# Kernel optimization log

Hardware: AMD Instinct MI355X
Metric: run time of the kernel (lower is better)

Reference implementation:

```python
import math
import jax, jax.numpy as jnp
import numpy as np

N_HEADS = 8

def setup_inputs() -> dict:
    key = jax.random.key(0)
    k1, k2 = jax.random.split(key)
    b, c, n = 8, 512, 2048  # c = n_heads * d = 8 * 64
    qkv = jax.random.normal(k1, (b, 3 * c, n), dtype=jnp.float32)
    mask = jax.random.uniform(k2, (b, n)) > 0.1
    return {"qkv": qkv, "mask": mask}

def reference(qkv, mask):
    b, width, n = qkv.shape
    m = N_HEADS
    assert width % (3 * m) == 0
    d = width // (3 * m)
    # 'b (m D) n -> (b m) D n' with D = 3d, then split into q, k, v
    x = qkv.reshape(b, m, 3 * d, n).reshape(b * m, 3 * d, n)
    q, k, v = x[:, :d], x[:, d:2 * d], x[:, 2 * d:]
    scale = 1.0 / math.sqrt(math.sqrt(d))
    # (B, i, j) attention logits, B = b*m
    weight = jnp.einsum('Bdi,Bdj->Bij', q * scale, k * scale)
    # mask: 'b j -> (b m) () j'
    mkey = jnp.broadcast_to(mask[:, None, None, :], (b, m, 1, n)).reshape(b * m, 1, n)
    neg = -jnp.finfo(weight.dtype).max
    weight = jnp.where(mkey, weight, neg)
    weight = jax.nn.softmax(weight, axis=-1)
    a = jnp.einsum('Bin,Bdn->Bdi', weight, v)  # (b*m, d, n)
    return a.reshape(b, m, d, n).reshape(b, m * d, n)
```

## Files before the change

### kernel.cpp

```cpp
#include <hip/hip_runtime.h>
#include <hip/hip_bf16.h>


typedef __attribute__((ext_vector_type(8))) short short8;
typedef __attribute__((ext_vector_type(4))) float f32x4;
typedef __attribute__((ext_vector_type(4))) unsigned int u32x4;

#define SEQ 2048
#define DH 64
#define NH 8
#define NHEADS_TOT 64
#define NTILES 32
#define TILE_BYTES 8192
#define IMG_MAT (NHEADS_TOT * NTILES * TILE_BYTES)
#define WS_NEED (3 * (size_t)IMG_MAT + 65536)
#define LOG2E 1.4426950408889634f
#define QSCALE (0.125f * LOG2E)

__device__ __forceinline__ unsigned short f2b(float f) {
  unsigned int u = __float_as_uint(f);
  u += 0x7FFFu + ((u >> 16) & 1u);
  return (unsigned short)(u >> 16);
}
__device__ __forceinline__ unsigned int pk2(float a, float b) {
  return (unsigned int)f2b(a) | ((unsigned int)f2b(b) << 16);
}
__device__ __forceinline__ unsigned int cvtpk(float lo, float hi) {
  unsigned int r;
  asm("v_cvt_pk_bf16_f32 %0, %1, %2" : "=v"(r) : "v"(lo), "v"(hi));
  return r;
}
union pkcast { u32x4 u; short8 s; };

__global__ __launch_bounds__(256)
void qkv_prep(const float* __restrict__ qkv, const void* __restrict__ mraw,
              char* __restrict__ ws) {
  __shared__ float Lf[64 * 68];
  __shared__ float mcol[64];
  __shared__ int flag;
  const int tid = threadIdx.x;
  const int b = blockIdx.x;

  if (b >= 3 * NHEADS_TOT * NTILES) {
    const int bi = b - 3 * NHEADS_TOT * NTILES;
    if (tid == 0) flag = 0;
    __syncthreads();
    const int* mi = (const int*)mraw;
    int bad = 0;
    for (int idx = tid; idx < 4096; idx += 256) {
      int v = mi[idx];
      bad |= (v != 0) & (v != 1);
    }
    if (bad) atomicOr(&flag, 1);
    __syncthreads();
    const bool isByte = (flag != 0);
    unsigned short* mo = (unsigned short*)(ws + 3 * (size_t)IMG_MAT) + bi * SEQ;
    for (int j = tid; j < SEQ; j += 256) {
      bool keep = isByte ? (((const unsigned char*)mraw)[bi * SEQ + j] != 0)
                         : (((const int*)mraw)[bi * SEQ + j] != 0);
      mo[j] = keep ? 0x3F80 : 0;
    }
    return;
  }

  const int m = b / (NHEADS_TOT * NTILES);
  const int rem = b - m * (NHEADS_TOT * NTILES);
  const int head = rem >> 5;
  const int t = rem & 31;
  const int bi = head >> 3, h = head & 7;
  const float* src = qkv + (size_t)bi * (3 * NH * DH * SEQ)
                         + (size_t)h * (3 * DH * SEQ)
                         + (size_t)m * (DH * SEQ);
  char* img = ws + (size_t)m * IMG_MAT + (size_t)(head * NTILES + t) * TILE_BYTES;

  if (m == 2) {
    if (tid == 0) flag = 0;
    __syncthreads();
    const int* mi = (const int*)mraw;
    int bad = 0;
    for (int idx = tid; idx < 4096; idx += 256) {
      int v = mi[idx];
      bad |= (v != 0) & (v != 1);
    }
    if (bad) atomicOr(&flag, 1);
    __syncthreads();
    const bool isByte = (flag != 0);
    if (tid < 64) {
      int j = t * 64 + tid;
      bool keep = isByte ? (((const unsigned char*)mraw)[bi * SEQ + j] != 0)
                         : (((const int*)mraw)[bi * SEQ + j] != 0);
      mcol[tid] = keep ? 1.0f : 0.0f;
    }
  }

  const float qs = (m == 0) ? QSCALE : 1.0f;
  const int trow = tid >> 4;
  const int tj4 = (tid & 15) * 4;
  #pragma unroll
  for (int p = 0; p < 4; ++p) {
    int dd = p * 16 + trow;
    float4 v = *(const float4*)(src + (size_t)dd * SEQ + t * 64 + tj4);
    v.x *= qs; v.y *= qs; v.z *= qs; v.w *= qs;
    *(float4*)(&Lf[dd * 68 + tj4]) = v;
  }
  __syncthreads();

  #pragma unroll
  for (int qq = 0; qq < 2; ++qq) {
    int q = tid * 2 + qq;
    int row = q >> 3;
    int cp = q & 7;
    int c = cp ^ (row & 7);
    unsigned int u[4];
    if (m == 2) {
      #pragma unroll
      for (int e2 = 0; e2 < 4; ++e2) {
        int cc = c * 8 + e2 * 2;
        float a = Lf[row * 68 + cc] * mcol[cc];
        float bb = Lf[row * 68 + cc + 1] * mcol[cc + 1];
        u[e2] = pk2(a, bb);
      }
    } else {
      #pragma unroll
      for (int e2 = 0; e2 < 4; ++e2) {
        float a = Lf[(c * 8 + e2 * 2) * 68 + row];
        float bb = Lf[(c * 8 + e2 * 2 + 1) * 68 + row];
        u[e2] = pk2(a, bb);
      }
    }
    u32x4 uv = { u[0], u[1], u[2], u[3] };
    *(u32x4*)(img + q * 16) = uv;
  }
}

#define KOFF 0
#define VOFF 16384
#define MOFF 32768
#define SMEMB 36864

__device__ __forceinline__ void async16(const void* g, void* l) {
  __builtin_amdgcn_global_load_lds(
      (const __attribute__((address_space(1))) void*)g,
      (__attribute__((address_space(3))) void*)l, 16, 0, 0);
}

__global__ __launch_bounds__(256, 4)
void qkv_attn2(const char* __restrict__ ws, float* __restrict__ out) {
  __shared__ __align__(16) char smem[SMEMB];
  const int tid = threadIdx.x;
  const int w = tid >> 6;
  const int lane = tid & 63;
  const int l15 = lane & 15;
  const int g = lane >> 4;
  const int l7 = l15 & 7;

  const int L = blockIdx.x;
  const int head = (L & 7) * 8 + ((L >> 3) >> 4);
  const int qblk = (L >> 3) & 15;
  const int bi = head >> 3, h = head & 7;

  const char* Qimg = ws + (size_t)(head * NTILES + qblk * 2) * TILE_BYTES;
  const char* Kimg = ws + (size_t)IMG_MAT + (size_t)(head * NTILES) * TILE_BYTES;
  const char* Vimg = ws + 2 * (size_t)IMG_MAT + (size_t)(head * NTILES) * TILE_BYTES;
  const char* m01g = ws + 3 * (size_t)IMG_MAT + (size_t)bi * (SEQ * 2);

  short8 qb[2][2];
  {
    const char* qt = Qimg + (w >> 1) * TILE_BYTES;
    const int rbase = (w & 1) * 32;
    #pragma unroll
    for (int mt = 0; mt < 2; ++mt)
      #pragma unroll
      for (int kk = 0; kk < 2; ++kk) {
        int row = rbase + mt * 16 + l15;
        int cp = (kk * 4 + g) ^ l7;
        qb[mt][kk] = *(const short8*)(qt + row * 128 + cp * 16);
      }
  }

  int kOff[4][2];
  #pragma unroll
  for (int f = 0; f < 4; ++f) {
    int row = 8 * (l15 >> 2) + (l15 & 3) + 4 * (f & 1) + 32 * (f >> 1);
    int r7 = row & 7;
    kOff[f][0] = row * 128 + (((0 + g) ^ r7) * 16);
    kOff[f][1] = row * 128 + (((4 + g) ^ r7) * 16);
  }
  int vOff[4][2];
  #pragma unroll
  for (int nt = 0; nt < 4; ++nt) {
    int vrow = nt * 16 + l15;
    vOff[nt][0] = vrow * 128 + (((0 + g) ^ l7) * 16);
    vOff[nt][1] = vrow * 128 + (((4 + g) ^ l7) * 16);
  }

  const int stOff = (w * 2 * 64 + lane) * 16;

  auto stage = [&](int buf, int tt) {
    const char* kt = Kimg + (size_t)tt * TILE_BYTES + stOff;
    const char* vt = Vimg + (size_t)tt * TILE_BYTES + stOff;
    char* kl = smem + KOFF + buf * 8192 + (w * 2) * 1024;
    char* vl = smem + VOFF + buf * 8192 + (w * 2) * 1024;
    async16(kt, kl);
    async16(kt + 1024, kl + 1024);
    async16(vt, vl);
    async16(vt + 1024, vl + 1024);
  };

  async16(m01g + w * 1024 + lane * 16, smem + MOFF + w * 1024);
  stage(0, 0);
  __syncthreads();

  f32x4 accO[2][4];
  #pragma unroll
  for (int mt = 0; mt < 2; ++mt)
    #pragma unroll
    for (int nt = 0; nt < 4; ++nt)
      accO[mt][nt] = (f32x4){0.f, 0.f, 0.f, 0.f};
  f32x4 accL[2];
  accL[0] = (f32x4){0.f, 0.f, 0.f, 0.f};
  accL[1] = (f32x4){0.f, 0.f, 0.f, 0.f};

  for (int t = 0; t < NTILES; ++t) {
    const int cur = t & 1;
    if (t + 1 < NTILES) stage(cur ^ 1, t + 1);

    const char* Kl = smem + KOFF + cur * 8192;
    f32x4 sAcc[2][4];
    __builtin_amdgcn_s_setprio(1);
    #pragma unroll
    for (int f = 0; f < 4; ++f) {
      short8 kb0 = *(const short8*)(Kl + kOff[f][0]);
      short8 kb1 = *(const short8*)(Kl + kOff[f][1]);
      #pragma unroll
      for (int mt = 0; mt < 2; ++mt) {
        f32x4 z = (f32x4){0.f, 0.f, 0.f, 0.f};
        z = __builtin_amdgcn_mfma_f32_16x16x32_bf16(kb0, qb[mt][0], z, 0, 0, 0);
        z = __builtin_amdgcn_mfma_f32_16x16x32_bf16(kb1, qb[mt][1], z, 0, 0, 0);
        sAcc[mt][f] = z;
      }
    }
    __builtin_amdgcn_s_setprio(0);

    short8 pa[2][2];
    #pragma unroll
    for (int mt = 0; mt < 2; ++mt) {
      float pv[4][4];
      #pragma unroll
      for (int f = 0; f < 4; ++f)
        #pragma unroll
        for (int r = 0; r < 4; ++r)
          pv[f][r] = __builtin_exp2f(sAcc[mt][f][r]);
      pkcast lo, hi;
      lo.u = (u32x4){ cvtpk(pv[0][0], pv[0][1]), cvtpk(pv[0][2], pv[0][3]),
                      cvtpk(pv[1][0], pv[1][1]), cvtpk(pv[1][2], pv[1][3]) };
      hi.u = (u32x4){ cvtpk(pv[2][0], pv[2][1]), cvtpk(pv[2][2], pv[2][3]),
                      cvtpk(pv[3][0], pv[3][1]), cvtpk(pv[3][2], pv[3][3]) };
      pa[mt][0] = lo.s;
      pa[mt][1] = hi.s;
    }

    const char* Ml = smem + MOFF + t * 128;
    short8 mf0 = *(const short8*)(Ml + g * 16);
    short8 mf1 = *(const short8*)(Ml + 64 + g * 16);
    #pragma unroll
    for (int mt = 0; mt < 2; ++mt) {
      accL[mt] = __builtin_amdgcn_mfma_f32_16x16x32_bf16(mf0, pa[mt][0], accL[mt], 0, 0, 0);
      accL[mt] = __builtin_amdgcn_mfma_f32_16x16x32_bf16(mf1, pa[mt][1], accL[mt], 0, 0, 0);
    }

    const char* Vl = smem + VOFF + cur * 8192;
    __builtin_amdgcn_s_setprio(1);
    #pragma unroll
    for (int nt = 0; nt < 4; ++nt) {
      short8 va0 = *(const short8*)(Vl + vOff[nt][0]);
      short8 va1 = *(const short8*)(Vl + vOff[nt][1]);
      #pragma unroll
      for (int mt = 0; mt < 2; ++mt) {
        accO[mt][nt] = __builtin_amdgcn_mfma_f32_16x16x32_bf16(va0, pa[mt][0], accO[mt][nt], 0, 0, 0);
        accO[mt][nt] = __builtin_amdgcn_mfma_f32_16x16x32_bf16(va1, pa[mt][1], accO[mt][nt], 0, 0, 0);
      }
    }
    __builtin_amdgcn_s_setprio(0);
    __syncthreads();
  }

  float* obase = out + (size_t)bi * (NH * DH * SEQ) + (size_t)h * (DH * SEQ);
  const int i0 = qblk * 128 + w * 32;
  #pragma unroll
  for (int mt = 0; mt < 2; ++mt) {
    float rl = 1.0f / accL[mt][0];
    int icol = i0 + mt * 16 + l15;
    #pragma unroll
    for (int nt = 0; nt < 4; ++nt)
      #pragma unroll
      for (int r = 0; r < 4; ++r) {
        int dd = nt * 16 + g * 4 + r;
        obase[(size_t)dd * SEQ + icol] = accO[mt][nt][r] * rl;
      }
  }
}

#define QT0 64
#define KT0 64
#define LDK0 72
#define OFF_QT0 0
#define OFF_KT0 9216
#define OFF_VL0 18432
#define OFF_P0  27648
#define OFF_MB0 36864
#define OFF_L0  37120
#define OFF_FLAG0 37376
#define SMEM_BYTES0 37408
#define NEG_BIG 3.0e38f

__device__ __forceinline__ float b2f(unsigned short s) {
  return __uint_as_float(((unsigned int)s) << 16);
}

__global__ __launch_bounds__(256, 2)
void qkv_attn_fused(const float* __restrict__ qkv,
                    const void* __restrict__ mraw,
                    float* __restrict__ out) {
  __shared__ __align__(16) char smem[SMEM_BYTES0];
  unsigned short* Qt = (unsigned short*)(smem + OFF_QT0);
  unsigned short* Kt = (unsigned short*)(smem + OFF_KT0);
  unsigned short* Vl = (unsigned short*)(smem + OFF_VL0);
  unsigned short* P  = (unsigned short*)(smem + OFF_P0);
  float* mb_lds = (float*)(smem + OFF_MB0);
  float* l_lds  = (float*)(smem + OFF_L0);
  int* flag = (int*)(smem + OFF_FLAG0);

  const int tid  = threadIdx.x;
  const int w    = tid >> 6;
  const int lane = tid & 63;
  const int l15  = lane & 15;
  const int g    = lane >> 4;
  const int dbase = g * 8;

  if (tid == 0) *flag = 0;
  __syncthreads();
  {
    const int* mi = (const int*)mraw;
    int bad = 0;
    for (int idx = tid; idx < 4096; idx += 256) {
      int v = mi[idx];
      bad |= (v != 0) & (v != 1);
    }
    if (bad) atomicOr(flag, 1);
  }
  __syncthreads();
  const bool maskIsByte = (*flag != 0);

  const int L = blockIdx.x;
  const int head  = (L & 7) * 8 + (L >> 8);
  const int qtile = (L >> 3) & 31;
  const int bi = head >> 3;
  const int h  = head & 7;
  const int i0 = qtile * QT0;

  const float* qbase = qkv + (size_t)bi * (3 * NH * DH * SEQ)
                           + (size_t)h * (3 * DH * SEQ);
  const float* kbase = qbase + DH * SEQ;
  const float* vbase = qbase + 2 * DH * SEQ;
  const unsigned char* mb8 = (const unsigned char*)mraw + (size_t)bi * SEQ;
  const int* mb32 = (const int*)mraw + (size_t)bi * SEQ;

  const int trow = tid >> 4;
  const int tj4  = (tid & 15) * 4;

  #pragma unroll
  for (int p = 0; p < 4; ++p) {
    int dd = p * 16 + trow;
    float4 v4 = *(const float4*)(qbase + (size_t)dd * SEQ + i0 + tj4);
    Qt[(tj4 + 0) * LDK0 + dd] = f2b(v4.x);
    Qt[(tj4 + 1) * LDK0 + dd] = f2b(v4.y);
    Qt[(tj4 + 2) * LDK0 + dd] = f2b(v4.z);
    Qt[(tj4 + 3) * LDK0 + dd] = f2b(v4.w);
  }
  __syncthreads();

  const short8 qa0 = *(const short8*)(&Qt[(w * 16 + l15) * LDK0 + dbase]);
  const short8 qa1 = *(const short8*)(&Qt[(w * 16 + l15) * LDK0 + 32 + dbase]);

  f32x4 accO[4];
  #pragma unroll
  for (int nt = 0; nt < 4; ++nt) accO[nt] = (f32x4){0.f, 0.f, 0.f, 0.f};
  float M[4], l[4];
  #pragma unroll
  for (int r = 0; r < 4; ++r) { M[r] = -NEG_BIG; l[r] = 0.0f; }

  for (int t = 0; t < (SEQ / KT0); ++t) {
    const int j0 = t * KT0;
    __syncthreads();

    #pragma unroll
    for (int p = 0; p < 4; ++p) {
      int dd = p * 16 + trow;
      float4 k4 = *(const float4*)(kbase + (size_t)dd * SEQ + j0 + tj4);
      Kt[(tj4 + 0) * LDK0 + dd] = f2b(k4.x);
      Kt[(tj4 + 1) * LDK0 + dd] = f2b(k4.y);
      Kt[(tj4 + 2) * LDK0 + dd] = f2b(k4.z);
      Kt[(tj4 + 3) * LDK0 + dd] = f2b(k4.w);
      float4 vv4 = *(const float4*)(vbase + (size_t)dd * SEQ + j0 + tj4);
      unsigned int lo = (unsigned int)f2b(vv4.x) | ((unsigned int)f2b(vv4.y) << 16);
      unsigned int hi = (unsigned int)f2b(vv4.z) | ((unsigned int)f2b(vv4.w) << 16);
      *(uint2*)(&Vl[dd * LDK0 + tj4]) = make_uint2(lo, hi);
    }
    if (tid < KT0) {
      int j = j0 + tid;
      bool keep = maskIsByte ? (mb8[j] != 0) : (mb32[j] != 0);
      mb_lds[tid] = keep ? 0.0f : -60000.0f;
    }
    __syncthreads();

    f32x4 sAcc[4];
    #pragma unroll
    for (int f = 0; f < 4; ++f) {
      f32x4 z = (f32x4){0.f, 0.f, 0.f, 0.f};
      short8 kb0 = *(const short8*)(&Kt[(f * 16 + l15) * LDK0 + dbase]);
      short8 kb1 = *(const short8*)(&Kt[(f * 16 + l15) * LDK0 + 32 + dbase]);
      z = __builtin_amdgcn_mfma_f32_16x16x32_bf16(qa0, kb0, z, 0, 0, 0);
      z = __builtin_amdgcn_mfma_f32_16x16x32_bf16(qa1, kb1, z, 0, 0, 0);
      sAcc[f] = z;
    }

    float mbf[4];
    #pragma unroll
    for (int f = 0; f < 4; ++f) mbf[f] = mb_lds[f * 16 + l15];

    float s[4][4];
    float rmax[4];
    #pragma unroll
    for (int r = 0; r < 4; ++r) rmax[r] = -NEG_BIG;
    #pragma unroll
    for (int f = 0; f < 4; ++f) {
      #pragma unroll
      for (int r = 0; r < 4; ++r) {
        s[f][r] = sAcc[f][r] * 0.125f + mbf[f];
        rmax[r] = fmaxf(rmax[r], s[f][r]);
      }
    }
    #pragma unroll
    for (int r = 0; r < 4; ++r) {
      rmax[r] = fmaxf(rmax[r], __shfl_xor(rmax[r], 1));
      rmax[r] = fmaxf(rmax[r], __shfl_xor(rmax[r], 2));
      rmax[r] = fmaxf(rmax[r], __shfl_xor(rmax[r], 4));
      rmax[r] = fmaxf(rmax[r], __shfl_xor(rmax[r], 8));
    }
    float alpha[4], newM[4];
    #pragma unroll
    for (int r = 0; r < 4; ++r) {
      newM[r] = fmaxf(M[r], rmax[r]);
      alpha[r] = __expf(M[r] - newM[r]);
      M[r] = newM[r];
    }
    unsigned short pb[4][4];
    float rsum[4] = {0.f, 0.f, 0.f, 0.f};
    #pragma unroll
    for (int f = 0; f < 4; ++f) {
      #pragma unroll
      for (int r = 0; r < 4; ++r) {
        float pvv = __expf(s[f][r] - newM[r]);
        unsigned short bb = f2b(pvv);
        pb[f][r] = bb;
        rsum[r] += b2f(bb);
      }
    }
    #pragma unroll
    for (int r = 0; r < 4; ++r) {
      rsum[r] += __shfl_xor(rsum[r], 1);
      rsum[r] += __shfl_xor(rsum[r], 2);
      rsum[r] += __shfl_xor(rsum[r], 4);
      rsum[r] += __shfl_xor(rsum[r], 8);
      l[r] = l[r] * alpha[r] + rsum[r];
    }
    #pragma unroll
    for (int nt = 0; nt < 4; ++nt) {
      #pragma unroll
      for (int r = 0; r < 4; ++r) accO[nt][r] *= alpha[r];
    }

    unsigned short* Pw = P + w * 16 * LDK0;
    #pragma unroll
    for (int f = 0; f < 4; ++f) {
      #pragma unroll
      for (int r = 0; r < 4; ++r)
        Pw[(g * 4 + r) * LDK0 + f * 16 + l15] = pb[f][r];
    }
    short8 pa0 = *(const short8*)(&Pw[l15 * LDK0 + dbase]);
    short8 pa1 = *(const short8*)(&Pw[l15 * LDK0 + 32 + dbase]);

    #pragma unroll
    for (int nt = 0; nt < 4; ++nt) {
      short8 vb0 = *(const short8*)(&Vl[(nt * 16 + l15) * LDK0 + dbase]);
      short8 vb1 = *(const short8*)(&Vl[(nt * 16 + l15) * LDK0 + 32 + dbase]);
      accO[nt] = __builtin_amdgcn_mfma_f32_16x16x32_bf16(pa0, vb0, accO[nt], 0, 0, 0);
      accO[nt] = __builtin_amdgcn_mfma_f32_16x16x32_bf16(pa1, vb1, accO[nt], 0, 0, 0);
    }
  }

  __syncthreads();
  float* O_lds = (float*)smem;
  #pragma unroll
  for (int nt = 0; nt < 4; ++nt) {
    #pragma unroll
    for (int r = 0; r < 4; ++r)
      O_lds[(w * 16 + g * 4 + r) * 68 + nt * 16 + l15] = accO[nt][r];
  }
  if (l15 == 0) {
    #pragma unroll
    for (int r = 0; r < 4; ++r) l_lds[w * 16 + g * 4 + r] = l[r];
  }
  __syncthreads();

  const int ti = tid & 63;
  const int td = tid >> 6;
  const float rl = 1.0f / l_lds[ti];
  float* obase = out + (size_t)bi * (NH * DH * SEQ)
                     + (size_t)h * (DH * SEQ) + i0 + ti;
  #pragma unroll
  for (int p = 0; p < 16; ++p) {
    int dd = p * 4 + td;
    obase[(size_t)dd * SEQ] = O_lds[ti * 68 + dd] * rl;
  }
}

extern "C" void kernel_launch(void* const* d_in, const int* in_sizes, int n_in,
                              void* d_out, int out_size, void* d_ws, size_t ws_size,
                              hipStream_t stream) {
  const float* qkv = (const float*)d_in[0];
  const void* mask = d_in[1];
  float* out = (float*)d_out;
  (void)in_sizes; (void)n_in; (void)out_size;

  if (ws_size >= WS_NEED && d_ws != nullptr) {
    char* ws = (char*)d_ws;
    qkv_prep<<<dim3(3 * NHEADS_TOT * NTILES + 8), dim3(256), 0, stream>>>(qkv, mask, ws);
    qkv_attn2<<<dim3(1024), dim3(256), 0, stream>>>(ws, out);
  } else {
    qkv_attn_fused<<<dim3(2048), dim3(256), 0, stream>>>(qkv, mask, out);
  }
}
```

Baseline: 120.2 us.

## Use two waves per block with 64 query rows each to reuse K/V fragments

The attention kernel now runs 128 threads (two waves) per block instead of four, and each wave handles 64 query rows (four M-tiles) rather than 32. Each K and V fragment read from LDS therefore feeds twice as many MFMAs, and the per-tile staging work is split across fewer waves. The QK, exp and P·V steps are also interleaved per M-tile. The cost is higher register pressure from doubled accumulators and Q fragments, and fewer waves per block to hide latency. Launch bounds drop to (128,2).

```diff
diff --git a/kernel.cpp b/kernel.cpp
--- a/kernel.cpp
+++ b/kernel.cpp
@@ -144,8 +144,8 @@
       (__attribute__((address_space(3))) void*)l, 16, 0, 0);
 }
 
-__global__ __launch_bounds__(256, 4)
-void qkv_attn2(const char* __restrict__ ws, float* __restrict__ out) {
+__global__ __launch_bounds__(128, 2)
+void qkv_attn3(const char* __restrict__ ws, float* __restrict__ out) {
   __shared__ __align__(16) char smem[SMEMB];
   const int tid = threadIdx.x;
   const int w = tid >> 6;
@@ -155,7 +155,7 @@
   const int l7 = l15 & 7;
 
   const int L = blockIdx.x;
-  const int head = (L & 7) * 8 + ((L >> 3) >> 4);
+  const int head = (L & 7) * 8 + (L >> 7);
   const int qblk = (L >> 3) & 15;
   const int bi = head >> 3, h = head & 7;
 
@@ -164,15 +164,14 @@
   const char* Vimg = ws + 2 * (size_t)IMG_MAT + (size_t)(head * NTILES) * TILE_BYTES;
   const char* m01g = ws + 3 * (size_t)IMG_MAT + (size_t)bi * (SEQ * 2);
 
-  short8 qb[2][2];
+  short8 qb[4][2];
   {
-    const char* qt = Qimg + (w >> 1) * TILE_BYTES;
-    const int rbase = (w & 1) * 32;
-    #pragma unroll
-    for (int mt = 0; mt < 2; ++mt)
+    const char* qt = Qimg + w * TILE_BYTES;
+    #pragma unroll
+    for (int mt = 0; mt < 4; ++mt)
       #pragma unroll
       for (int kk = 0; kk < 2; ++kk) {
-        int row = rbase + mt * 16 + l15;
+        int row = mt * 16 + l15;
         int cp = (kk * 4 + g) ^ l7;
         qb[mt][kk] = *(const short8*)(qt + row * 128 + cp * 16);
       }
@@ -194,63 +193,69 @@
     vOff[nt][1] = vrow * 128 + (((4 + g) ^ l7) * 16);
   }
 
-  const int stOff = (w * 2 * 64 + lane) * 16;
+  const int stOff = (w * 4 * 64 + lane) * 16;
 
   auto stage = [&](int buf, int tt) {
     const char* kt = Kimg + (size_t)tt * TILE_BYTES + stOff;
     const char* vt = Vimg + (size_t)tt * TILE_BYTES + stOff;
-    char* kl = smem + KOFF + buf * 8192 + (w * 2) * 1024;
-    char* vl = smem + VOFF + buf * 8192 + (w * 2) * 1024;
-    async16(kt, kl);
-    async16(kt + 1024, kl + 1024);
-    async16(vt, vl);
-    async16(vt + 1024, vl + 1024);
+    char* kl = smem + KOFF + buf * 8192 + (w * 4) * 1024;
+    char* vl = smem + VOFF + buf * 8192 + (w * 4) * 1024;
+    #pragma unroll
+    for (int c = 0; c < 4; ++c) {
+      async16(kt + c * 1024, kl + c * 1024);
+      async16(vt + c * 1024, vl + c * 1024);
+    }
   };
 
-  async16(m01g + w * 1024 + lane * 16, smem + MOFF + w * 1024);
+  async16(m01g + w * 2048 + lane * 16, smem + MOFF + w * 2048);
+  async16(m01g + w * 2048 + 1024 + lane * 16, smem + MOFF + w * 2048 + 1024);
   stage(0, 0);
   __syncthreads();
 
-  f32x4 accO[2][4];
-  #pragma unroll
-  for (int mt = 0; mt < 2; ++mt)
+  f32x4 accO[4][4];
+  #pragma unroll
+  for (int mt = 0; mt < 4; ++mt)
     #pragma unroll
     for (int nt = 0; nt < 4; ++nt)
       accO[mt][nt] = (f32x4){0.f, 0.f, 0.f, 0.f};
-  f32x4 accL[2];
-  accL[0] = (f32x4){0.f, 0.f, 0.f, 0.f};
-  accL[1] = (f32x4){0.f, 0.f, 0.f, 0.f};
+  f32x4 accL[4];
+  #pragma unroll
+  for (int mt = 0; mt < 4; ++mt) accL[mt] = (f32x4){0.f, 0.f, 0.f, 0.f};
 
   for (int t = 0; t < NTILES; ++t) {
     const int cur = t & 1;
     if (t + 1 < NTILES) stage(cur ^ 1, t + 1);
 
     const char* Kl = smem + KOFF + cur * 8192;
-    f32x4 sAcc[2][4];
-    __builtin_amdgcn_s_setprio(1);
+    short8 kb[4][2];
     #pragma unroll
     for (int f = 0; f < 4; ++f) {
-      short8 kb0 = *(const short8*)(Kl + kOff[f][0]);
-      short8 kb1 = *(const short8*)(Kl + kOff[f][1]);
-      #pragma unroll
-      for (int mt = 0; mt < 2; ++mt) {
+      kb[f][0] = *(const short8*)(Kl + kOff[f][0]);
+      kb[f][1] = *(const short8*)(Kl + kOff[f][1]);
+    }
+    const char* Ml = smem + MOFF + t * 128;
+    short8 mf0 = *(const short8*)(Ml + g * 16);
+    short8 mf1 = *(const short8*)(Ml + 64 + g * 16);
+
+    short8 pa[4][2];
+    #pragma unroll
+    for (int mt = 0; mt < 4; ++mt) {
+      f32x4 sA[4];
+      __builtin_amdgcn_s_setprio(1);
+      #pragma unroll
+      for (int f = 0; f < 4; ++f) {
         f32x4 z = (f32x4){0.f, 0.f, 0.f, 0.f};
-        z = __builtin_amdgcn_mfma_f32_16x16x32_bf16(kb0, qb[mt][0], z, 0, 0, 0);
-        z = __builtin_amdgcn_mfma_f32_16x16x32_bf16(kb1, qb[mt][1], z, 0, 0, 0);
-        sAcc[mt][f] = z;
-      }
-    }
-    __builtin_amdgcn_s_setprio(0);
-
-    short8 pa[2][2];
-    #pragma unroll
-    for (int mt = 0; mt < 2; ++mt) {
+        z = __builtin_amdgcn_mfma_f32_16x16x32_bf16(kb[f][0], qb[mt][0], z, 0, 0, 0);
+        z = __builtin_amdgcn_mfma_f32_16x16x32_bf16(kb[f][1], qb[mt][1], z, 0, 0, 0);
+        sA[f] = z;
+      }
+      __builtin_amdgcn_s_setprio(0);
       float pv[4][4];
       #pragma unroll
       for (int f = 0; f < 4; ++f)
         #pragma unroll
         for (int r = 0; r < 4; ++r)
-          pv[f][r] = __builtin_exp2f(sAcc[mt][f][r]);
+          pv[f][r] = __builtin_exp2f(sA[f][r]);
       pkcast lo, hi;
       lo.u = (u32x4){ cvtpk(pv[0][0], pv[0][1]), cvtpk(pv[0][2], pv[0][3]),
                       cvtpk(pv[1][0], pv[1][1]), cvtpk(pv[1][2], pv[1][3]) };
@@ -258,13 +263,6 @@
                       cvtpk(pv[3][0], pv[3][1]), cvtpk(pv[3][2], pv[3][3]) };
       pa[mt][0] = lo.s;
       pa[mt][1] = hi.s;
-    }
-
-    const char* Ml = smem + MOFF + t * 128;
-    short8 mf0 = *(const short8*)(Ml + g * 16);
-    short8 mf1 = *(const short8*)(Ml + 64 + g * 16);
-    #pragma unroll
-    for (int mt = 0; mt < 2; ++mt) {
       accL[mt] = __builtin_amdgcn_mfma_f32_16x16x32_bf16(mf0, pa[mt][0], accL[mt], 0, 0, 0);
       accL[mt] = __builtin_amdgcn_mfma_f32_16x16x32_bf16(mf1, pa[mt][1], accL[mt], 0, 0, 0);
     }
@@ -276,7 +274,7 @@
       short8 va0 = *(const short8*)(Vl + vOff[nt][0]);
       short8 va1 = *(const short8*)(Vl + vOff[nt][1]);
       #pragma unroll
-      for (int mt = 0; mt < 2; ++mt) {
+      for (int mt = 0; mt < 4; ++mt) {
         accO[mt][nt] = __builtin_amdgcn_mfma_f32_16x16x32_bf16(va0, pa[mt][0], accO[mt][nt], 0, 0, 0);
         accO[mt][nt] = __builtin_amdgcn_mfma_f32_16x16x32_bf16(va1, pa[mt][1], accO[mt][nt], 0, 0, 0);
       }
@@ -286,9 +284,9 @@
   }
 
   float* obase = out + (size_t)bi * (NH * DH * SEQ) + (size_t)h * (DH * SEQ);
-  const int i0 = qblk * 128 + w * 32;
-  #pragma unroll
-  for (int mt = 0; mt < 2; ++mt) {
+  const int i0 = qblk * 128 + w * 64;
+  #pragma unroll
+  for (int mt = 0; mt < 4; ++mt) {
     float rl = 1.0f / accL[mt][0];
     int icol = i0 + mt * 16 + l15;
     #pragma unroll
@@ -537,7 +535,7 @@
   if (ws_size >= WS_NEED && d_ws != nullptr) {
     char* ws = (char*)d_ws;
     qkv_prep<<<dim3(3 * NHEADS_TOT * NTILES + 8), dim3(256), 0, stream>>>(qkv, mask, ws);
-    qkv_attn2<<<dim3(1024), dim3(256), 0, stream>>>(ws, out);
+    qkv_attn3<<<dim3(1024), dim3(128), 0, stream>>>(ws, out);
   } else {
     qkv_attn_fused<<<dim3(2048), dim3(256), 0, stream>>>(qkv, mask, out);
   }
```

After: 129.7 us. 8.0% more time.
